# Kernel optimization log

Hardware: AMD Instinct MI355X
Metric: run time of the kernel (lower is better)

The kernel has to match this reference:

```python
import jax, jax.numpy as jnp
import numpy as np

GRID_SIZE = 5
SPLINE_ORDER = 3
GRID_MIN = -1.0
GRID_MAX = 1.0
H = (GRID_MAX - GRID_MIN) / GRID_SIZE          # grid interval
G0 = GRID_MIN - SPLINE_ORDER * H               # first (extended) knot = grid[:,0]


def _basis_matrix():
    # Uniform B-spline power-basis matrix, same recurrence as the torch code.
    M = np.array([[1.0]], dtype=np.float64)
    scalar = 1.0
    for k in range(2, SPLINE_ORDER + 2):
        t1 = np.pad(M, ((0, 1), (0, 0)))
        t3 = np.pad(M, ((1, 0), (0, 0)))
        t2 = np.zeros((k - 1, k))
        t4 = np.zeros((k - 1, k))
        for i in range(k - 1):
            t2[i, i] = i + 1
            t2[i, i + 1] = k - (i + 2)
            t4[i, i] = -1.0
            t4[i, i + 1] = 1.0
        M = t1 @ t2 + t3 @ t4
        scalar *= 1.0 / (k - 1)
    return (M * scalar).astype(np.float32)

BASIS = jnp.asarray(_basis_matrix())  # (spline_order+1, spline_order+1)


def setup_inputs():
    key = jax.random.key(0)
    k1, k2, k3 = jax.random.split(key, 3)
    N, FIN, FOUT = 2048, 128, 128
    x = jax.random.normal(k1, (N, FIN), dtype=jnp.float32)
    base_weight = jax.random.normal(k2, (FOUT, FIN), dtype=jnp.float32) * 0.1
    spline_weight = jax.random.normal(k3, (FIN, FOUT, GRID_SIZE + SPLINE_ORDER), dtype=jnp.float32) * 0.1
    return {"x": x, "base_weight": base_weight, "spline_weight": spline_weight}


def _forward(x, base_weight, spline_weight):
    N, fin = x.shape
    fout = base_weight.shape[0]
    k = SPLINE_ORDER
    # base branch: SiLU activation then linear
    base_out = jax.nn.silu(x) @ base_weight.T                       # (N, fout)
    # input normalization: Hardtanh around grid center (shift=0, scale=1 for [-1,1])
    shift = (GRID_MIN + GRID_MAX) / 2.0
    scale = (GRID_MAX - GRID_MIN) / 2.0
    xn = jnp.clip((x - shift) / scale, -1.0, 1.0) * scale + shift
    # bucketize: bin index + fractional position (replaces floor/compare + torch.nonzero)
    t = (xn - G0) / H
    fl = jnp.floor(t)
    u1 = t - fl                                                     # (x - interval_floor) / interval
    idx = jnp.clip(fl.astype(jnp.int32), k, k + GRID_SIZE - 1)      # clamped knot-interval index
    cfloor = idx - k                                                # (N, fin) first control point index
    # power bases [1, u, u^2, ..., u^k] -> b-spline basis via basis matrix
    pows = u1[..., None] ** jnp.arange(k + 1, dtype=x.dtype)        # (N, fin, k+1)
    bspl = pows @ BASIS.astype(x.dtype)                             # (N, fin, k+1)
    # faithful to torch: spline_weight.view(out, in, -1) memory reinterpretation
    cp = jnp.reshape(spline_weight, (fout, fin, GRID_SIZE + k))
    gidx = cfloor[..., None] + jnp.arange(k + 1)                    # (N, fin, k+1) control point indices
    i_idx = jnp.arange(fin)[None, :, None]
    gathered = cp[:, i_idx, gidx]                                   # (fout, N, fin, k+1)
    gathered = jnp.transpose(gathered, (1, 0, 2, 3))                # (N, fout, fin, k+1)
    # faithful to torch: .view(N, in, k+1, out) memory reinterpretation
    cpr = jnp.reshape(gathered, (N, fin, k + 1, fout))
    # per-feature spline matmul then sum over in_features (KAN aggregation)
    spline_out = jnp.einsum('nij,nijo->no', bspl, cpr)              # (N, fout)
    return base_out + spline_out


def reference(x, base_weight, spline_weight):
    return _forward(x, base_weight, spline_weight)
```

## Files before the change

### kernel.cpp

```cpp
#include <hip/hip_runtime.h>
#include <hip/hip_bf16.h>
#include <math.h>

typedef __attribute__((ext_vector_type(8))) short short8;
typedef __attribute__((ext_vector_type(4))) float floatx4;

static __device__ __forceinline__ unsigned short bfbits(float f) {
    __hip_bfloat16 h = __float2bfloat16(f);
    unsigned short u;
    __builtin_memcpy(&u, &h, 2);
    return u;
}
static __device__ __forceinline__ unsigned pack2(float lo, float hi) {
    return (unsigned)bfbits(lo) | ((unsigned)bfbits(hi) << 16);
}

#define SP_STR  136
#define SBN_STR 76
#define SBB_STR 136
#define ST_STR  68
#define SC_STR  132

__global__ __launch_bounds__(256, 3) void kan_fused(
    const float* __restrict__ x,
    const float* __restrict__ bw,
    const float* __restrict__ sw,
    float* __restrict__ out)
{
    __shared__ short sP[5 * 16 * SP_STR];
    __shared__ short sBn[128 * SBN_STR];
    __shared__ float sT[2][16 * ST_STR];
    __shared__ unsigned char sC[16 * SC_STR];

    const int tid = threadIdx.x;
    const int nb  = blockIdx.x >> 2;
    const int s   = blockIdx.x & 3;
    const int n0  = nb * 16;

    const int ar = tid >> 4;
    const int sg = tid & 15;

    const int r  = tid >> 4;
    const int i0 = (tid & 15) * 8;
    float v[8];
    *(float4*)(v)     = *(const float4*)(x + (n0 + r) * 128 + i0);
    *(float4*)(v + 4) = *(const float4*)(x + (n0 + r) * 128 + i0 + 4);

    float4 pre[4];
#pragma unroll
    for (int rr = 0; rr < 4; ++rr)
        pre[rr] = *(const float4*)(sw + (ar + 16 * rr) * 1024 + s * 64 + sg * 4);

    {
        float A5[5][8];
        unsigned char cc8[8];
#pragma unroll
        for (int i = 0; i < 8; ++i) {
            float xv = v[i];
            float si = xv / (1.0f + expf(-xv));
            float xn = fminf(fmaxf(xv, -1.0f), 1.0f);
            float t  = (xn + 2.2f) / 0.4f;
            float u  = t - floorf(t);
            int idx  = (int)floorf(t);
            idx = min(max(idx, 3), 7);
            cc8[i] = (unsigned char)(idx - 3);
            float u2 = u * u, u3 = u2 * u, om = 1.0f - u;
            A5[0][i] = om * om * om * (1.0f / 6.0f);
            A5[1][i] = 0.5f * u3 - u2 + (2.0f / 3.0f);
            A5[2][i] = -0.5f * u3 + 0.5f * u2 + 0.5f * u + (1.0f / 6.0f);
            A5[3][i] = u3 * (1.0f / 6.0f);
            A5[4][i] = si;
        }
#pragma unroll
        for (int g = 0; g < 5; ++g) {
            unsigned p0 = pack2(A5[g][0], A5[g][1]);
            unsigned p1 = pack2(A5[g][2], A5[g][3]);
            unsigned p2 = pack2(A5[g][4], A5[g][5]);
            unsigned p3 = pack2(A5[g][6], A5[g][7]);
            *(uint4*)(&sP[(g * 16 + r) * SP_STR + i0]) = make_uint4(p0, p1, p2, p3);
        }
        *(unsigned*)(&sC[r * SC_STR + i0])     = cc8[0] | (cc8[1]<<8) | (cc8[2]<<16) | (cc8[3]<<24);
        *(unsigned*)(&sC[r * SC_STR + i0 + 4]) = cc8[4] | (cc8[5]<<8) | (cc8[6]<<16) | (cc8[7]<<24);
    }

#pragma unroll
    for (int rr = 0; rr < 4; ++rr)
        *(uint2*)(&sBn[(ar + 16 * rr) * SBN_STR + sg * 4]) =
            make_uint2(pack2(pre[rr].x, pre[rr].y), pack2(pre[rr].z, pre[rr].w));
#pragma unroll
    for (int rr = 4; rr < 8; ++rr) {
        float4 h = *(const float4*)(sw + (ar + 16 * rr) * 1024 + s * 64 + sg * 4);
        *(uint2*)(&sBn[(ar + 16 * rr) * SBN_STR + sg * 4]) =
            make_uint2(pack2(h.x, h.y), pack2(h.z, h.w));
    }
    __syncthreads();

    const int w = tid >> 6, l = tid & 63;
    const int m = l & 15, q = l >> 4;
    const int gn  = tid >> 4;
    const int go2 = tid & 15;
    const int oh  = 8 * s + (go2 >> 1);
    const int oloc = 8 * (go2 >> 1) + 2 * (go2 & 1);

    float racc0 = 0.f, racc1 = 0.f;
    float4 bpre[4];

#pragma unroll
    for (int t = 0; t < 4; ++t) {
        const int p = t & 1;

        if (t < 3) {
#pragma unroll
            for (int rr = 0; rr < 4; ++rr)
                pre[rr] = *(const float4*)(sw + (ar + 16 * rr) * 1024 + (s + 4 * (t + 1)) * 64 + sg * 4);
        } else {
#pragma unroll
            for (int i = 0; i < 4; ++i) {
                int e = i * 256 + tid;
                bpre[i] = *(const float4*)(bw + (32 * s + (e >> 5)) * 128 + (e & 31) * 4);
            }
        }

        if (t > 0) {
            int c   = sC[gn * SC_STR + 32 * (t - 1) + oh];
            int rel = oloc + c;
            racc0 += sT[1 - p][gn * ST_STR + rel];
            racc1 += sT[1 - p][gn * ST_STR + rel + 1];
        }

        floatx4 acc = {0.f, 0.f, 0.f, 0.f};
#pragma unroll
        for (int kk = 0; kk < 4; ++kk) {
            short8 af = *(const short8*)(&sP[(t * 16 + m) * SP_STR + q * 8 + kk * 32]);
            short8 bf;
#pragma unroll
            for (int j2 = 0; j2 < 8; ++j2)
                bf[j2] = sBn[(kk * 32 + q * 8 + j2) * SBN_STR + 16 * w + m];
            acc = __builtin_amdgcn_mfma_f32_16x16x32_bf16(af, bf, acc, 0, 0, 0);
        }
#pragma unroll
        for (int rr = 0; rr < 4; ++rr)
            sT[p][(q * 4 + rr) * ST_STR + 16 * w + m] = acc[rr];

        __syncthreads();

        if (t < 3) {
#pragma unroll
            for (int rr = 0; rr < 4; ++rr)
                *(uint2*)(&sBn[(ar + 16 * rr) * SBN_STR + sg * 4]) =
                    make_uint2(pack2(pre[rr].x, pre[rr].y), pack2(pre[rr].z, pre[rr].w));
#pragma unroll
            for (int rr = 4; rr < 8; ++rr) {
                float4 h = *(const float4*)(sw + (ar + 16 * rr) * 1024 + (s + 4 * (t + 1)) * 64 + sg * 4);
                *(uint2*)(&sBn[(ar + 16 * rr) * SBN_STR + sg * 4]) =
                    make_uint2(pack2(h.x, h.y), pack2(h.z, h.w));
            }
        } else {
#pragma unroll
            for (int i = 0; i < 4; ++i) {
                int e = i * 256 + tid;
                *(uint2*)(&sBn[(e >> 5) * SBB_STR + (e & 31) * 4]) =
                    make_uint2(pack2(bpre[i].x, bpre[i].y), pack2(bpre[i].z, bpre[i].w));
            }
        }
        __syncthreads();
    }

    if (w < 2) {
        floatx4 acc = {0.f, 0.f, 0.f, 0.f};
#pragma unroll
        for (int kk = 0; kk < 4; ++kk) {
            short8 af = *(const short8*)(&sP[(4 * 16 + m) * SP_STR + q * 8 + kk * 32]);
            short8 bf = *(const short8*)(&sBn[(16 * w + m) * SBB_STR + q * 8 + kk * 32]);
            acc = __builtin_amdgcn_mfma_f32_16x16x32_bf16(af, bf, acc, 0, 0, 0);
        }
#pragma unroll
        for (int rr = 0; rr < 4; ++rr)
            sT[0][(q * 4 + rr) * ST_STR + 16 * w + m] = acc[rr];
    }
    __syncthreads();

    {
        int c   = sC[gn * SC_STR + 32 * 3 + oh];
        int rel = oloc + c;
        racc0 += sT[1][gn * ST_STR + rel];
        racc1 += sT[1][gn * ST_STR + rel + 1];
    }
    racc0 += sT[0][gn * ST_STR + 2 * go2];
    racc1 += sT[0][gn * ST_STR + 2 * go2 + 1];

    *(float2*)(out + (n0 + gn) * 128 + 32 * s + 2 * go2) = make_float2(racc0, racc1);
}

extern "C" void kernel_launch(void* const* d_in, const int* in_sizes, int n_in,
                              void* d_out, int out_size, void* d_ws, size_t ws_size,
                              hipStream_t stream) {
    const float* x  = (const float*)d_in[0];
    const float* bw = (const float*)d_in[1];
    const float* sw = (const float*)d_in[2];
    float* out = (float*)d_out;
    kan_fused<<<dim3(512), dim3(256), 0, stream>>>(x, bw, sw, out);
}
```

Measured before the change: 64.68 us.

## Process spline weights in two wide phases with deeper register prefetch

The four 64-column spline-weight stages are merged into two 128-column stages. Each stage issues two MFMAs per wave, and 16 float4 loads per thread are prefetched into registers, where the old code loaded 4 early and 4 late. This halves the number of stage barriers and gives global loads more time in flight. In exchange, register and LDS use grow, and launch bounds drop from 3 to 2 blocks per SM, which lowers occupancy.

```diff
diff --git a/kernel.cpp b/kernel.cpp
--- a/kernel.cpp
+++ b/kernel.cpp
@@ -16,12 +16,12 @@
 }
 
 #define SP_STR  136
-#define SBN_STR 76
+#define SBN_STR 132
 #define SBB_STR 136
-#define ST_STR  68
+#define STW     132
 #define SC_STR  132
 
-__global__ __launch_bounds__(256, 3) void kan_fused(
+__global__ __launch_bounds__(256, 2) void kan_fused(
     const float* __restrict__ x,
     const float* __restrict__ bw,
     const float* __restrict__ sw,
@@ -29,7 +29,7 @@
 {
     __shared__ short sP[5 * 16 * SP_STR];
     __shared__ short sBn[128 * SBN_STR];
-    __shared__ float sT[2][16 * ST_STR];
+    __shared__ float sT[2][16 * STW];
     __shared__ unsigned char sC[16 * SC_STR];
 
     const int tid = threadIdx.x;
@@ -46,10 +46,12 @@
     *(float4*)(v)     = *(const float4*)(x + (n0 + r) * 128 + i0);
     *(float4*)(v + 4) = *(const float4*)(x + (n0 + r) * 128 + i0 + 4);
 
-    float4 pre[4];
-#pragma unroll
-    for (int rr = 0; rr < 4; ++rr)
-        pre[rr] = *(const float4*)(sw + (ar + 16 * rr) * 1024 + s * 64 + sg * 4);
+    float4 pf[16];
+#pragma unroll
+    for (int h = 0; h < 2; ++h)
+#pragma unroll
+        for (int aa = 0; aa < 8; ++aa)
+            pf[h * 8 + aa] = *(const float4*)(sw + (ar + 16 * aa) * 1024 + (s + 4 * h) * 64 + sg * 4);
 
     {
         float A5[5][8];
@@ -84,87 +86,117 @@
     }
 
 #pragma unroll
-    for (int rr = 0; rr < 4; ++rr)
-        *(uint2*)(&sBn[(ar + 16 * rr) * SBN_STR + sg * 4]) =
-            make_uint2(pack2(pre[rr].x, pre[rr].y), pack2(pre[rr].z, pre[rr].w));
-#pragma unroll
-    for (int rr = 4; rr < 8; ++rr) {
-        float4 h = *(const float4*)(sw + (ar + 16 * rr) * 1024 + s * 64 + sg * 4);
-        *(uint2*)(&sBn[(ar + 16 * rr) * SBN_STR + sg * 4]) =
-            make_uint2(pack2(h.x, h.y), pack2(h.z, h.w));
-    }
+    for (int h = 0; h < 2; ++h)
+#pragma unroll
+        for (int aa = 0; aa < 8; ++aa) {
+            float4 w4 = pf[h * 8 + aa];
+            *(uint2*)(&sBn[(ar + 16 * aa) * SBN_STR + 64 * h + sg * 4]) =
+                make_uint2(pack2(w4.x, w4.y), pack2(w4.z, w4.w));
+        }
     __syncthreads();
 
     const int w = tid >> 6, l = tid & 63;
     const int m = l & 15, q = l >> 4;
-    const int gn  = tid >> 4;
-    const int go2 = tid & 15;
-    const int oh  = 8 * s + (go2 >> 1);
+    const int gn   = tid >> 4;
+    const int go2  = tid & 15;
+    const int oh   = 8 * s + (go2 >> 1);
     const int oloc = 8 * (go2 >> 1) + 2 * (go2 & 1);
 
     float racc0 = 0.f, racc1 = 0.f;
     float4 bpre[4];
 
 #pragma unroll
-    for (int t = 0; t < 4; ++t) {
-        const int p = t & 1;
-
-        if (t < 3) {
-#pragma unroll
-            for (int rr = 0; rr < 4; ++rr)
-                pre[rr] = *(const float4*)(sw + (ar + 16 * rr) * 1024 + (s + 4 * (t + 1)) * 64 + sg * 4);
-        } else {
-#pragma unroll
-            for (int i = 0; i < 4; ++i) {
-                int e = i * 256 + tid;
-                bpre[i] = *(const float4*)(bw + (32 * s + (e >> 5)) * 128 + (e & 31) * 4);
+    for (int h = 0; h < 2; ++h)
+#pragma unroll
+        for (int aa = 0; aa < 8; ++aa)
+            pf[h * 8 + aa] = *(const float4*)(sw + (ar + 16 * aa) * 1024 + (s + 8 + 4 * h) * 64 + sg * 4);
+
+    {
+        floatx4 acc0 = {0.f,0.f,0.f,0.f}, acc1 = {0.f,0.f,0.f,0.f};
+#pragma unroll
+        for (int kk = 0; kk < 4; ++kk) {
+            short8 af = *(const short8*)(&sP[(0 * 16 + m) * SP_STR + q * 8 + kk * 32]);
+            short8 af1 = *(const short8*)(&sP[(1 * 16 + m) * SP_STR + q * 8 + kk * 32]);
+            short8 b0, b1;
+#pragma unroll
+            for (int j2 = 0; j2 < 8; ++j2) {
+                b0[j2] = sBn[(kk * 32 + q * 8 + j2) * SBN_STR + 32 * w + m];
+                b1[j2] = sBn[(kk * 32 + q * 8 + j2) * SBN_STR + 32 * w + 16 + m];
             }
-        }
-
-        if (t > 0) {
-            int c   = sC[gn * SC_STR + 32 * (t - 1) + oh];
-            int rel = oloc + c;
-            racc0 += sT[1 - p][gn * ST_STR + rel];
-            racc1 += sT[1 - p][gn * ST_STR + rel + 1];
-        }
-
-        floatx4 acc = {0.f, 0.f, 0.f, 0.f};
+            short8 aL = (32 * w < 64) ? af : af1;
+            short8 aR = (32 * w + 16 < 64) ? af : af1;
+            acc0 = __builtin_amdgcn_mfma_f32_16x16x32_bf16(aL, b0, acc0, 0, 0, 0);
+            acc1 = __builtin_amdgcn_mfma_f32_16x16x32_bf16(aR, b1, acc1, 0, 0, 0);
+        }
+#pragma unroll
+        for (int rr = 0; rr < 4; ++rr) {
+            sT[0][(q * 4 + rr) * STW + 32 * w + m]      = acc0[rr];
+            sT[0][(q * 4 + rr) * STW + 32 * w + 16 + m] = acc1[rr];
+        }
+    }
+    __syncthreads();
+
+#pragma unroll
+    for (int h = 0; h < 2; ++h)
+#pragma unroll
+        for (int aa = 0; aa < 8; ++aa) {
+            float4 w4 = pf[h * 8 + aa];
+            *(uint2*)(&sBn[(ar + 16 * aa) * SBN_STR + 64 * h + sg * 4]) =
+                make_uint2(pack2(w4.x, w4.y), pack2(w4.z, w4.w));
+        }
+#pragma unroll
+    for (int h = 0; h < 2; ++h) {
+        int c   = sC[gn * SC_STR + 32 * h + oh];
+        int rel = 64 * h + oloc + c;
+        racc0 += sT[0][gn * STW + rel];
+        racc1 += sT[0][gn * STW + rel + 1];
+    }
+    __syncthreads();
+
+#pragma unroll
+    for (int i = 0; i < 4; ++i) {
+        int e = i * 256 + tid;
+        bpre[i] = *(const float4*)(bw + (32 * s + (e >> 5)) * 128 + (e & 31) * 4);
+    }
+    {
+        floatx4 acc0 = {0.f,0.f,0.f,0.f}, acc1 = {0.f,0.f,0.f,0.f};
 #pragma unroll
         for (int kk = 0; kk < 4; ++kk) {
-            short8 af = *(const short8*)(&sP[(t * 16 + m) * SP_STR + q * 8 + kk * 32]);
-            short8 bf;
-#pragma unroll
-            for (int j2 = 0; j2 < 8; ++j2)
-                bf[j2] = sBn[(kk * 32 + q * 8 + j2) * SBN_STR + 16 * w + m];
-            acc = __builtin_amdgcn_mfma_f32_16x16x32_bf16(af, bf, acc, 0, 0, 0);
-        }
-#pragma unroll
-        for (int rr = 0; rr < 4; ++rr)
-            sT[p][(q * 4 + rr) * ST_STR + 16 * w + m] = acc[rr];
-
-        __syncthreads();
-
-        if (t < 3) {
-#pragma unroll
-            for (int rr = 0; rr < 4; ++rr)
-                *(uint2*)(&sBn[(ar + 16 * rr) * SBN_STR + sg * 4]) =
-                    make_uint2(pack2(pre[rr].x, pre[rr].y), pack2(pre[rr].z, pre[rr].w));
-#pragma unroll
-            for (int rr = 4; rr < 8; ++rr) {
-                float4 h = *(const float4*)(sw + (ar + 16 * rr) * 1024 + (s + 4 * (t + 1)) * 64 + sg * 4);
-                *(uint2*)(&sBn[(ar + 16 * rr) * SBN_STR + sg * 4]) =
-                    make_uint2(pack2(h.x, h.y), pack2(h.z, h.w));
+            short8 af2 = *(const short8*)(&sP[(2 * 16 + m) * SP_STR + q * 8 + kk * 32]);
+            short8 af3 = *(const short8*)(&sP[(3 * 16 + m) * SP_STR + q * 8 + kk * 32]);
+            short8 b0, b1;
+#pragma unroll
+            for (int j2 = 0; j2 < 8; ++j2) {
+                b0[j2] = sBn[(kk * 32 + q * 8 + j2) * SBN_STR + 32 * w + m];
+                b1[j2] = sBn[(kk * 32 + q * 8 + j2) * SBN_STR + 32 * w + 16 + m];
             }
-        } else {
-#pragma unroll
-            for (int i = 0; i < 4; ++i) {
-                int e = i * 256 + tid;
-                *(uint2*)(&sBn[(e >> 5) * SBB_STR + (e & 31) * 4]) =
-                    make_uint2(pack2(bpre[i].x, bpre[i].y), pack2(bpre[i].z, bpre[i].w));
-            }
-        }
-        __syncthreads();
-    }
+            short8 aL = (32 * w < 64) ? af2 : af3;
+            short8 aR = (32 * w + 16 < 64) ? af2 : af3;
+            acc0 = __builtin_amdgcn_mfma_f32_16x16x32_bf16(aL, b0, acc0, 0, 0, 0);
+            acc1 = __builtin_amdgcn_mfma_f32_16x16x32_bf16(aR, b1, acc1, 0, 0, 0);
+        }
+#pragma unroll
+        for (int rr = 0; rr < 4; ++rr) {
+            sT[1][(q * 4 + rr) * STW + 32 * w + m]      = acc0[rr];
+            sT[1][(q * 4 + rr) * STW + 32 * w + 16 + m] = acc1[rr];
+        }
+    }
+    __syncthreads();
+
+#pragma unroll
+    for (int i = 0; i < 4; ++i) {
+        int e = i * 256 + tid;
+        *(uint2*)(&sBn[(e >> 5) * SBB_STR + (e & 31) * 4]) =
+            make_uint2(pack2(bpre[i].x, bpre[i].y), pack2(bpre[i].z, bpre[i].w));
+    }
+#pragma unroll
+    for (int h = 0; h < 2; ++h) {
+        int c   = sC[gn * SC_STR + 32 * (2 + h) + oh];
+        int rel = 64 * h + oloc + c;
+        racc0 += sT[1][gn * STW + rel];
+        racc1 += sT[1][gn * STW + rel + 1];
+    }
+    __syncthreads();
 
     if (w < 2) {
         floatx4 acc = {0.f, 0.f, 0.f, 0.f};
@@ -176,18 +208,12 @@
         }
 #pragma unroll
         for (int rr = 0; rr < 4; ++rr)
-            sT[0][(q * 4 + rr) * ST_STR + 16 * w + m] = acc[rr];
-    }
-    __syncthreads();
-
-    {
-        int c   = sC[gn * SC_STR + 32 * 3 + oh];
-        int rel = oloc + c;
-        racc0 += sT[1][gn * ST_STR + rel];
-        racc1 += sT[1][gn * ST_STR + rel + 1];
-    }
-    racc0 += sT[0][gn * ST_STR + 2 * go2];
-    racc1 += sT[0][gn * ST_STR + 2 * go2 + 1];
+            sT[0][(q * 4 + rr) * STW + 16 * w + m] = acc[rr];
+    }
+    __syncthreads();
+
+    racc0 += sT[0][gn * STW + 2 * go2];
+    racc1 += sT[0][gn * STW + 2 * go2 + 1];
 
     *(float2*)(out + (n0 + gn) * 128 + 32 * s + 2 * go2) = make_float2(racc0, racc1);
 }
```

Measured after the change: 65.23 us. About the same (+0.8%).
